# Kernel optimization log

Measured on AMD Instinct MI355X. Metric: run time of the kernel, lower is better.

## Reference

```python
import jax, jax.numpy as jnp
import numpy as np

DIM = 768
NUM_HEADS = 12
HEAD_DIM = DIM // NUM_HEADS
B, V, L = 1, 8, 512


def _block_mask_bias(V, L, dtype):
    # allowed[v_q, v_k]: views 0,1 attend to views 0,1 (incl. self); views >=2 causal (v_q >= v_k)
    vq = jnp.arange(V)[:, None]
    vk = jnp.arange(V)[None, :]
    allowed = ((vq <= 1) & (vk <= 1)) | (vq >= vk)  # [V, V]
    allowed = jnp.repeat(jnp.repeat(allowed, L, axis=0), L, axis=1)  # [V*L, V*L]
    neg_inf = jnp.asarray(-jnp.inf, dtype)
    return jnp.where(allowed, jnp.asarray(0.0, dtype), neg_inf)


def setup_inputs() -> dict:
    key = jax.random.key(0)
    k0, k1, k2, k3, k4, k5 = jax.random.split(key, 6)
    s = 1.0 / np.sqrt(DIM)
    x = jax.random.normal(k0, (B, V, L, DIM), dtype=jnp.float32)
    Wq = jax.random.normal(k1, (DIM, DIM), dtype=jnp.float32) * s
    Wk = jax.random.normal(k2, (DIM, DIM), dtype=jnp.float32) * s
    Wv = jax.random.normal(k3, (DIM, DIM), dtype=jnp.float32) * s
    Wo = jax.random.normal(k4, (DIM, DIM), dtype=jnp.float32) * s
    bo = jax.random.normal(k5, (DIM,), dtype=jnp.float32) * 0.01
    return {"x": x, "Wq": Wq, "Wk": Wk, "Wv": Wv, "Wo": Wo, "bo": bo}


def reference(x, Wq, Wk, Wv, Wo, bo):
    Bx, Vx, Lx, C = x.shape
    S = Vx * Lx
    H, D = NUM_HEADS, HEAD_DIM
    scale = D ** -0.5

    xf = x.reshape(Bx, S, C)
    # linear projections (no bias, qkv_bias=False), split heads -> [B, H, S, D]
    def split_heads(t):
        return t.reshape(Bx, S, H, D).transpose(0, 2, 1, 3)
    q = split_heads(xf @ Wq.T)
    k = split_heads(xf @ Wk.T)
    v = split_heads(xf @ Wv.T)

    bias = _block_mask_bias(Vx, Lx, q.dtype)  # [S, S], broadcast over B, H
    scores = jnp.einsum("bhqd,bhkd->bhqk", q, k) * scale + bias
    attn = jax.nn.softmax(scores, axis=-1)
    out = jnp.einsum("bhqk,bhkd->bhqd", attn, v)  # [B, H, S, D]
    out = out.transpose(0, 2, 1, 3).reshape(Bx, Vx, Lx, C)
    return out @ Wo.T + bo
```

## Files before the change

kernel.cpp:

```cpp
#include <hip/hip_runtime.h>

#define S_TOT 4096
#define C_DIM 768
#define QKV_LD 2304
#define NH 12
#define QSCALE 0.18033688011112042f

using f32x4  = __attribute__((ext_vector_type(4))) float;
using bf16x8 = __attribute__((ext_vector_type(8))) __bf16;

#if __has_builtin(__builtin_amdgcn_exp2f)
#define EXP2(x) __builtin_amdgcn_exp2f(x)
#else
#define EXP2(x) exp2f(x)
#endif

#define DRAIN_AND_BARRIER()                                     \
  do {                                                          \
    asm volatile("s_waitcnt vmcnt(0) lgkmcnt(0)" ::: "memory"); \
    __builtin_amdgcn_sched_barrier(0);                          \
    __syncthreads();                                            \
  } while (0)

__device__ inline unsigned short f2bf_bits(float f) {
  unsigned int u = __float_as_uint(f);
  u = (u + 0x7FFFu + ((u >> 16) & 1u)) >> 16;
  return (unsigned short)u;
}
__device__ inline __bf16 f2bf(float f) {
  unsigned short s = f2bf_bits(f);
  __bf16 b;
  __builtin_memcpy(&b, &s, 2);
  return b;
}

__device__ __forceinline__ void gl_lds16(const __bf16* g, __bf16* l) {
  __builtin_amdgcn_global_load_lds(
      (__attribute__((address_space(1))) void*)(g),
      (__attribute__((address_space(3))) void*)(l), 16, 0, 0);
}

__global__ void cvt_all(const float* __restrict__ x, const float* __restrict__ Wq,
                        const float* __restrict__ Wk, const float* __restrict__ Wv,
                        const float* __restrict__ Wo, __bf16* __restrict__ dst) {
  const int XN = S_TOT * C_DIM;
  const int WN = C_DIM * C_DIM;
  int i = (blockIdx.x * blockDim.x + threadIdx.x) * 4;
  if (i >= XN + 4 * WN) return;
  const float* src; float scale = 1.f; int off;
  if (i < XN)               { src = x;  off = i; }
  else if (i < XN + WN)     { src = Wq; off = i - XN; scale = QSCALE; }
  else if (i < XN + 2 * WN) { src = Wk; off = i - XN - WN; }
  else if (i < XN + 3 * WN) { src = Wv; off = i - XN - 2 * WN; }
  else                      { src = Wo; off = i - XN - 3 * WN; }
  float4 v = *reinterpret_cast<const float4*>(src + off);
  ushort4 o;
  o.x = f2bf_bits(v.x * scale); o.y = f2bf_bits(v.y * scale);
  o.z = f2bf_bits(v.z * scale); o.w = f2bf_bits(v.w * scale);
  *reinterpret_cast<ushort4*>(reinterpret_cast<unsigned short*>(dst) + i) = o;
}

template<bool OUT_BIAS_F32, bool SPLIT_V>
__global__ __launch_bounds__(256) void gemm128(
    const __bf16* __restrict__ A, const __bf16* __restrict__ B,
    void* __restrict__ Cv, const float* __restrict__ bias,
    __bf16* __restrict__ VtOut, int K, int ldc) {
  __shared__ __bf16 As[128][64];
  __shared__ __bf16 Bs[128][64];
  const int t = threadIdx.x, lane = t & 63, wv = t >> 6;
  const int wr = wv >> 1, wc = wv & 1;
  const int lhi = lane >> 4, llo = lane & 15;
  const int m0 = blockIdx.y * 128, n0 = blockIdx.x * 128;

  f32x4 acc[4][4];
  #pragma unroll
  for (int a = 0; a < 4; ++a)
    #pragma unroll
    for (int b = 0; b < 4; ++b) acc[a][b] = (f32x4){0.f, 0.f, 0.f, 0.f};

  for (int kt = 0; kt < K; kt += 64) {
    __syncthreads();
    #pragma unroll
    for (int n = 0; n < 4; ++n) {
      const int ci = n * 256 + wv * 64 + lane;
      const int r = ci >> 3;
      const int cc = (ci & 7) ^ (r & 7);
      gl_lds16(A + (size_t)(m0 + r) * K + kt + cc * 8, &As[0][0] + ci * 8);
      gl_lds16(B + (size_t)(n0 + r) * K + kt + cc * 8, &Bs[0][0] + ci * 8);
    }
    DRAIN_AND_BARRIER();
    #pragma unroll
    for (int kk = 0; kk < 2; ++kk) {
      bf16x8 af[4], bfr[4];
      #pragma unroll
      for (int mi = 0; mi < 4; ++mi) {
        const int row = wr * 64 + mi * 16 + llo;
        af[mi] = *reinterpret_cast<const bf16x8*>(
            &As[0][0] + row * 64 + (((kk << 2) | lhi) ^ (llo & 7)) * 8);
      }
      #pragma unroll
      for (int ni = 0; ni < 4; ++ni) {
        const int row = wc * 64 + ni * 16 + llo;
        bfr[ni] = *reinterpret_cast<const bf16x8*>(
            &Bs[0][0] + row * 64 + (((kk << 2) | lhi) ^ (llo & 7)) * 8);
      }
      #pragma unroll
      for (int mi = 0; mi < 4; ++mi)
        #pragma unroll
        for (int ni = 0; ni < 4; ++ni)
          acc[mi][ni] = __builtin_amdgcn_mfma_f32_16x16x32_bf16(af[mi], bfr[ni], acc[mi][ni], 0, 0, 0);
    }
  }

  if (SPLIT_V && n0 >= 1536) {
    const int head = (n0 - 1536 + wc * 64) >> 6;
    const int tile64 = (m0 >> 6) + wr;
    #pragma unroll
    for (int mi = 0; mi < 4; ++mi) {
      const int p = (mi >> 1) * 32 + lhi * 8 + (mi & 1) * 4;
      #pragma unroll
      for (int ni = 0; ni < 4; ++ni) {
        const int d = ni * 16 + llo;
        ushort4 o;
        o.x = f2bf_bits(acc[mi][ni][0]); o.y = f2bf_bits(acc[mi][ni][1]);
        o.z = f2bf_bits(acc[mi][ni][2]); o.w = f2bf_bits(acc[mi][ni][3]);
        uint2 u; __builtin_memcpy(&u, &o, 8);
        *reinterpret_cast<uint2*>(VtOut + ((size_t)head * 64 + d) * S_TOT + tile64 * 64 + p) = u;
      }
    }
    return;
  }

  #pragma unroll
  for (int mi = 0; mi < 4; ++mi)
    #pragma unroll
    for (int ni = 0; ni < 4; ++ni)
      #pragma unroll
      for (int i = 0; i < 4; ++i) {
        const int row = m0 + wr * 64 + mi * 16 + lhi * 4 + i;
        const int col = n0 + wc * 64 + ni * 16 + llo;
        if constexpr (OUT_BIAS_F32) {
          reinterpret_cast<float*>(Cv)[(size_t)row * ldc + col] = acc[mi][ni][i] + bias[col];
        } else {
          reinterpret_cast<__bf16*>(Cv)[(size_t)row * ldc + col] = f2bf(acc[mi][ni][i]);
        }
      }
}

__device__ __forceinline__ void decode9(int j, int& qb64, int& h, int& half, bool& split) {
  if (j < 192)      { split = true;  half = j & 1;  qb64 = 56 + ((j >> 1) & 7); h = j >> 4; }
  else if (j < 288) { int k = j - 192; split = false; half = 0; qb64 = 24 + (k & 7); h = k >> 3; }
  else if (j < 480) { int k = j - 288; split = true;  half = k & 1; qb64 = 48 + ((k >> 1) & 7); h = k >> 4; }
  else if (j < 672) { int k = j - 480; split = true;  half = k & 1; qb64 = 40 + ((k >> 1) & 7); h = k >> 4; }
  else if (j < 768) { int k = j - 672; split = false; half = 0; qb64 = 16 + (k & 7); h = k >> 3; }
  else if (j < 960) { int k = j - 768; split = true;  half = k & 1; qb64 = 32 + ((k >> 1) & 7); h = k >> 4; }
  else              { int k = j - 960; split = false; half = 0; qb64 = k & 15; h = k >> 4; }
}

__global__ __launch_bounds__(256) void attn_fused9(
    const __bf16* __restrict__ QKV, const __bf16* __restrict__ Vtp,
    __bf16* __restrict__ att, float* __restrict__ Opart,
    float* __restrict__ lpart) {
  __shared__ __bf16 Ks[3][64][64];
  __shared__ __bf16 Vs[3][64][64];
  const int t = threadIdx.x, lane = t & 63, wv = t >> 6;
  const int llo = lane & 15, hi = lane >> 4;
  const int sw = llo & 7;
  int qb64, h, half; bool split;
  decode9((int)blockIdx.x, qb64, h, half, split);
  const int vq = qb64 >> 3;
  const int kv_end = (vq <= 1) ? 1024 : (vq + 1) * 512;
  const int n_tiles = split ? (kv_end >> 7) : (kv_end >> 6);
  const int kstart = split ? half * (kv_end >> 1) : 0;
  const int q0 = qb64 * 64;
  const int myq = q0 + wv * 16 + llo;

  bf16x8 qf[2];
  {
    const __bf16* qrow = QKV + (size_t)myq * QKV_LD + h * 64;
    qf[0] = *reinterpret_cast<const bf16x8*>(qrow + hi * 8);
    qf[1] = *reinterpret_cast<const bf16x8*>(qrow + 32 + hi * 8);
  }
  asm volatile("s_waitcnt vmcnt(0)" ::: "memory");

  f32x4 Oa[4];
  #pragma unroll
  for (int dt = 0; dt < 4; ++dt) Oa[dt] = (f32x4){0.f, 0.f, 0.f, 0.f};
  float l = 0.f;

  const int ci0 = (wv * 2 + 0) * 64 + lane, r0 = ci0 >> 3, c0 = (ci0 & 7) ^ (r0 & 7);
  const int ci1 = (wv * 2 + 1) * 64 + lane, r1 = ci1 >> 3, c1 = (ci1 & 7) ^ (r1 & 7);
  const __bf16* kp0 = QKV + (size_t)(kstart + r0) * QKV_LD + C_DIM + h * 64 + c0 * 8;
  const __bf16* kp1 = QKV + (size_t)(kstart + r1) * QKV_LD + C_DIM + h * 64 + c1 * 8;
  const __bf16* vp0 = Vtp + ((size_t)h * 64 + r0) * S_TOT + kstart + c0 * 8;
  const __bf16* vp1 = Vtp + ((size_t)h * 64 + r1) * S_TOT + kstart + c1 * 8;
  __bf16* const kd0 = &Ks[0][0][0] + ci0 * 8 - lane * 8;
  __bf16* const kd1 = &Ks[0][0][0] + ci1 * 8 - lane * 8;
  __bf16* const vd0 = &Vs[0][0][0] + ci0 * 8 - lane * 8;
  __bf16* const vd1 = &Vs[0][0][0] + ci1 * 8 - lane * 8;

  auto stage = [&](int buf) {
    const size_t bo = (size_t)buf * 4096;
    gl_lds16(kp0, kd0 + bo);
    gl_lds16(vp0, vd0 + bo);
    gl_lds16(kp1, kd1 + bo);
    gl_lds16(vp1, vd1 + bo);
    kp0 += (size_t)64 * QKV_LD; kp1 += (size_t)64 * QKV_LD;
    vp0 += 64; vp1 += 64;
  };

  stage(0);
  stage(1);
  int cur = 0;
  for (int tt = 0; tt < n_tiles; ++tt) {
    if (tt + 1 < n_tiles) {
      asm volatile("s_waitcnt vmcnt(4)" ::: "memory");
    } else {
      asm volatile("s_waitcnt vmcnt(0)" ::: "memory");
    }
    __builtin_amdgcn_sched_barrier(0);
    __builtin_amdgcn_s_barrier();
    __builtin_amdgcn_sched_barrier(0);
    if (tt + 2 < n_tiles) {
      const int nxt = (cur + 2 >= 3) ? cur - 1 : cur + 2;
      stage(nxt);
    }
    const __bf16* Kb = &Ks[cur][0][0];
    const __bf16* Vb = &Vs[cur][0][0];

    f32x4 sc[4];
    #pragma unroll
    for (int nt = 0; nt < 4; ++nt) sc[nt] = (f32x4){0.f, 0.f, 0.f, 0.f};
    #pragma unroll
    for (int nt = 0; nt < 4; ++nt) {
      const __bf16* kr = Kb + (nt * 16 + llo) * 64;
      bf16x8 kf0 = *reinterpret_cast<const bf16x8*>(kr + ((hi ^ sw) * 8));
      bf16x8 kf1 = *reinterpret_cast<const bf16x8*>(kr + (((4 + hi) ^ sw) * 8));
      sc[nt] = __builtin_amdgcn_mfma_f32_16x16x32_bf16(kf0, qf[0], sc[nt], 0, 0, 0);
      sc[nt] = __builtin_amdgcn_mfma_f32_16x16x32_bf16(kf1, qf[1], sc[nt], 0, 0, 0);
    }

    float pp[4][4];
    #pragma unroll
    for (int nt = 0; nt < 4; ++nt)
      #pragma unroll
      for (int i = 0; i < 4; ++i) pp[nt][i] = EXP2(sc[nt][i]);
    float t0 = (pp[0][0] + pp[0][1]) + (pp[0][2] + pp[0][3]);
    float t1 = (pp[1][0] + pp[1][1]) + (pp[1][2] + pp[1][3]);
    float t2 = (pp[2][0] + pp[2][1]) + (pp[2][2] + pp[2][3]);
    float t3 = (pp[3][0] + pp[3][1]) + (pp[3][2] + pp[3][3]);
    l += (t0 + t1) + (t2 + t3);

    bf16x8 pf[2];
    #pragma unroll
    for (int mm = 0; mm < 2; ++mm)
      #pragma unroll
      for (int jj = 0; jj < 8; ++jj)
        pf[mm][jj] = (__bf16)pp[2 * mm + (jj >> 2)][jj & 3];

    #pragma unroll
    for (int dt = 0; dt < 4; ++dt) {
      const __bf16* vr = Vb + (dt * 16 + llo) * 64;
      #pragma unroll
      for (int mm = 0; mm < 2; ++mm) {
        bf16x8 va = *reinterpret_cast<const bf16x8*>(vr + (((mm * 4 + hi) ^ sw) * 8));
        Oa[dt] = __builtin_amdgcn_mfma_f32_16x16x32_bf16(va, pf[mm], Oa[dt], 0, 0, 0);
      }
    }
    cur = (cur + 1 == 3) ? 0 : cur + 1;
  }

  l += __shfl_xor(l, 16);
  l += __shfl_xor(l, 32);
  if (!split) {
    const float inv = 1.f / l;
    #pragma unroll
    for (int dt = 0; dt < 4; ++dt) {
      ushort4 o;
      o.x = f2bf_bits(Oa[dt][0] * inv);
      o.y = f2bf_bits(Oa[dt][1] * inv);
      o.z = f2bf_bits(Oa[dt][2] * inv);
      o.w = f2bf_bits(Oa[dt][3] * inv);
      *reinterpret_cast<ushort4*>(att + (size_t)myq * C_DIM + h * 64 + dt * 16 + hi * 4) = o;
    }
  } else {
    const int slot = ((qb64 - 32) * 12 + h) * 2 + half;
    float* Ob = Opart + (((size_t)slot * 64) + wv * 16 + llo) * 64;
    #pragma unroll
    for (int dt = 0; dt < 4; ++dt)
      *reinterpret_cast<f32x4*>(Ob + dt * 16 + hi * 4) = Oa[dt];
    if (hi == 0) lpart[slot * 64 + wv * 16 + llo] = l;
  }
}

__global__ __launch_bounds__(256) void merge9(
    const float* __restrict__ Opart, const float* __restrict__ lpart,
    __bf16* __restrict__ att) {
  const int b = blockIdx.x;
  const int qi = b / 12, h = b - qi * 12;
  const int t = threadIdx.x;
  const int r = t >> 2, d0 = (t & 3) * 16;
  const int slot0 = b * 2;
  const float* O0 = Opart + ((size_t)slot0 * 64 + r) * 64 + d0;
  const float* O1 = Opart + ((size_t)(slot0 + 1) * 64 + r) * 64 + d0;
  const float linv = 1.f / (lpart[slot0 * 64 + r] + lpart[(slot0 + 1) * 64 + r]);
  __bf16* dst = att + ((size_t)(qi + 32) * 64 + r) * C_DIM + h * 64 + d0;
  #pragma unroll
  for (int i = 0; i < 4; ++i) {
    f32x4 a = *reinterpret_cast<const f32x4*>(O0 + i * 4);
    f32x4 c = *reinterpret_cast<const f32x4*>(O1 + i * 4);
    ushort4 o;
    o.x = f2bf_bits((a[0] + c[0]) * linv);
    o.y = f2bf_bits((a[1] + c[1]) * linv);
    o.z = f2bf_bits((a[2] + c[2]) * linv);
    o.w = f2bf_bits((a[3] + c[3]) * linv);
    *reinterpret_cast<ushort4*>(dst + i * 4) = o;
  }
}

extern "C" void kernel_launch(void* const* d_in, const int* in_sizes, int n_in,
                              void* d_out, int out_size, void* d_ws, size_t ws_size,
                              hipStream_t stream) {
  const float* x  = (const float*)d_in[0];
  const float* Wq = (const float*)d_in[1];
  const float* Wk = (const float*)d_in[2];
  const float* Wv = (const float*)d_in[3];
  const float* Wo = (const float*)d_in[4];
  const float* bo = (const float*)d_in[5];

  __bf16* xb   = (__bf16*)d_ws;
  __bf16* Wqkv = xb + (size_t)S_TOT * C_DIM;
  __bf16* Wob  = Wqkv + (size_t)3 * C_DIM * C_DIM;
  __bf16* QKV  = Wob + (size_t)C_DIM * C_DIM;
  __bf16* Vtp  = QKV + (size_t)S_TOT * QKV_LD;
  __bf16* att  = Vtp + (size_t)NH * 64 * S_TOT;
  float*  Opart = (float*)(att + (size_t)S_TOT * C_DIM);
  float*  lpart = Opart + (size_t)768 * 64 * 64;

  {
    const int tot = S_TOT * C_DIM + 4 * C_DIM * C_DIM;
    cvt_all<<<dim3((tot / 4 + 255) / 256), dim3(256), 0, stream>>>(
        x, Wq, Wk, Wv, Wo, xb);
  }

  gemm128<false, true><<<dim3(QKV_LD / 128, S_TOT / 128), dim3(256), 0, stream>>>(
      xb, Wqkv, (void*)QKV, nullptr, Vtp, C_DIM, QKV_LD);

  attn_fused9<<<dim3(1152), dim3(256), 0, stream>>>(QKV, Vtp, att, Opart, lpart);

  merge9<<<dim3(384), dim3(256), 0, stream>>>(Opart, lpart, att);

  gemm128<true, false><<<dim3(C_DIM / 128, S_TOT / 128), dim3(256), 0, stream>>>(
      att, Wob, d_out, bo, nullptr, C_DIM, C_DIM);
}
```

Measured before the change: 101.2 us.

## Rebalance attention split-KV work and load V fragments directly from global

Replaces the two-way KV split with a finer partition so every query block, not only the later views, is split into chunks of roughly 12-16 KV tiles, raising the attention grid from 1152 to 1920 blocks. The V projection is written in a pre-swizzled fragment layout so each lane reads its MFMA operands straight from global memory into registers, dropping the V LDS staging buffer and half of the async copies. The merge kernel now combines 2-4 partials per query block. This trades more partial-output traffic and a larger merge for better load balance and lower LDS use, with V reads now exposed to global latency inside the loop.

```diff
diff --git a/kernel.cpp b/kernel.cpp
--- a/kernel.cpp
+++ b/kernel.cpp
@@ -64,7 +64,7 @@
 __global__ __launch_bounds__(256) void gemm128(
     const __bf16* __restrict__ A, const __bf16* __restrict__ B,
     void* __restrict__ Cv, const float* __restrict__ bias,
-    __bf16* __restrict__ VtOut, int K, int ldc) {
+    __bf16* __restrict__ V2, int K, int ldc) {
   __shared__ __bf16 As[128][64];
   __shared__ __bf16 Bs[128][64];
   const int t = threadIdx.x, lane = t & 63, wv = t >> 6;
@@ -114,10 +114,10 @@
 
   if (SPLIT_V && n0 >= 1536) {
     const int head = (n0 - 1536 + wc * 64) >> 6;
-    const int tile64 = (m0 >> 6) + wr;
+    const int T = (m0 >> 6) + wr;
     #pragma unroll
     for (int mi = 0; mi < 4; ++mi) {
-      const int p = (mi >> 1) * 32 + lhi * 8 + (mi & 1) * 4;
+      const int c = (mi >> 1) * 4 + lhi;
       #pragma unroll
       for (int ni = 0; ni < 4; ++ni) {
         const int d = ni * 16 + llo;
@@ -125,7 +125,8 @@
         o.x = f2bf_bits(acc[mi][ni][0]); o.y = f2bf_bits(acc[mi][ni][1]);
         o.z = f2bf_bits(acc[mi][ni][2]); o.w = f2bf_bits(acc[mi][ni][3]);
         uint2 u; __builtin_memcpy(&u, &o, 8);
-        *reinterpret_cast<uint2*>(VtOut + ((size_t)head * 64 + d) * S_TOT + tile64 * 64 + p) = u;
+        *reinterpret_cast<uint2*>(
+            V2 + ((((size_t)head * 64 + T) * 8 + c) * 64 + d) * 8 + (mi & 1) * 4) = u;
       }
     }
     return;
@@ -147,31 +148,49 @@
       }
 }
 
-__device__ __forceinline__ void decode9(int j, int& qb64, int& h, int& half, bool& split) {
-  if (j < 192)      { split = true;  half = j & 1;  qb64 = 56 + ((j >> 1) & 7); h = j >> 4; }
-  else if (j < 288) { int k = j - 192; split = false; half = 0; qb64 = 24 + (k & 7); h = k >> 3; }
-  else if (j < 480) { int k = j - 288; split = true;  half = k & 1; qb64 = 48 + ((k >> 1) & 7); h = k >> 4; }
-  else if (j < 672) { int k = j - 480; split = true;  half = k & 1; qb64 = 40 + ((k >> 1) & 7); h = k >> 4; }
-  else if (j < 768) { int k = j - 672; split = false; half = 0; qb64 = 16 + (k & 7); h = k >> 3; }
-  else if (j < 960) { int k = j - 768; split = true;  half = k & 1; qb64 = 32 + ((k >> 1) & 7); h = k >> 4; }
-  else              { int k = j - 960; split = false; half = 0; qb64 = k & 15; h = k >> 4; }
-}
-
-__global__ __launch_bounds__(256) void attn_fused9(
-    const __bf16* __restrict__ QKV, const __bf16* __restrict__ Vtp,
+__device__ __forceinline__ void decode10(int j, int& qb64, int& h, int& nt,
+                                         int& kstart, int& slot) {
+  if (j < 384) {
+    const int c = j & 3, q = (j >> 2) & 7; h = j >> 5;
+    qb64 = 56 + q; nt = 16; kstart = c * 1024;
+    slot = ((q * 12) + h) * 4 + c;
+  } else if (j < 672) {
+    const int k = j - 384, c = k % 3, k3 = k / 3, q = k3 & 7; h = k3 >> 3;
+    qb64 = 40 + q; nt = 16; kstart = c * 1024;
+    slot = 768 + ((q * 12) + h) * 3 + c;
+  } else if (j < 864) {
+    const int k = j - 672, c = k & 1, q = (k >> 1) & 7; h = k >> 4;
+    qb64 = 24 + q; nt = 16; kstart = c * 1024;
+    slot = 1344 + ((q * 12) + h) * 2 + c;
+  } else if (j < 1056) {
+    const int k = j - 864;
+    qb64 = k & 15; h = k >> 4; nt = 16; kstart = 0; slot = -1;
+  } else if (j < 1440) {
+    const int k = j - 1056, c = k & 3, q = (k >> 2) & 7; h = k >> 5;
+    qb64 = 48 + q; nt = 14; kstart = c * 896;
+    slot = 384 + ((q * 12) + h) * 4 + c;
+  } else if (j < 1728) {
+    const int k = j - 1440, c = k % 3, k3 = k / 3, q = k3 & 7; h = k3 >> 3;
+    qb64 = 32 + q; nt = (c == 0) ? 14 : 13;
+    kstart = (c == 0) ? 0 : (896 + (c - 1) * 832);
+    slot = 1056 + ((q * 12) + h) * 3 + c;
+  } else {
+    const int k = j - 1728, c = k & 1, q = (k >> 1) & 7; h = k >> 4;
+    qb64 = 16 + q; nt = 12; kstart = c * 768;
+    slot = 1536 + ((q * 12) + h) * 2 + c;
+  }
+}
+
+__global__ __launch_bounds__(256) void attn_fused10(
+    const __bf16* __restrict__ QKV, const __bf16* __restrict__ V2,
     __bf16* __restrict__ att, float* __restrict__ Opart,
     float* __restrict__ lpart) {
   __shared__ __bf16 Ks[3][64][64];
-  __shared__ __bf16 Vs[3][64][64];
   const int t = threadIdx.x, lane = t & 63, wv = t >> 6;
   const int llo = lane & 15, hi = lane >> 4;
   const int sw = llo & 7;
-  int qb64, h, half; bool split;
-  decode9((int)blockIdx.x, qb64, h, half, split);
-  const int vq = qb64 >> 3;
-  const int kv_end = (vq <= 1) ? 1024 : (vq + 1) * 512;
-  const int n_tiles = split ? (kv_end >> 7) : (kv_end >> 6);
-  const int kstart = split ? half * (kv_end >> 1) : 0;
+  int qb64, h, n_tiles, kstart, slot;
+  decode10((int)blockIdx.x, qb64, h, n_tiles, kstart, slot);
   const int q0 = qb64 * 64;
   const int myq = q0 + wv * 16 + llo;
 
@@ -192,41 +211,44 @@
   const int ci1 = (wv * 2 + 1) * 64 + lane, r1 = ci1 >> 3, c1 = (ci1 & 7) ^ (r1 & 7);
   const __bf16* kp0 = QKV + (size_t)(kstart + r0) * QKV_LD + C_DIM + h * 64 + c0 * 8;
   const __bf16* kp1 = QKV + (size_t)(kstart + r1) * QKV_LD + C_DIM + h * 64 + c1 * 8;
-  const __bf16* vp0 = Vtp + ((size_t)h * 64 + r0) * S_TOT + kstart + c0 * 8;
-  const __bf16* vp1 = Vtp + ((size_t)h * 64 + r1) * S_TOT + kstart + c1 * 8;
-  __bf16* const kd0 = &Ks[0][0][0] + ci0 * 8 - lane * 8;
-  __bf16* const kd1 = &Ks[0][0][0] + ci1 * 8 - lane * 8;
-  __bf16* const vd0 = &Vs[0][0][0] + ci0 * 8 - lane * 8;
-  __bf16* const vd1 = &Vs[0][0][0] + ci1 * 8 - lane * 8;
+  __bf16* const kd0 = &Ks[0][0][0] + (wv * 2 + 0) * 512;
+  __bf16* const kd1 = &Ks[0][0][0] + (wv * 2 + 1) * 512;
 
   auto stage = [&](int buf) {
     const size_t bo = (size_t)buf * 4096;
     gl_lds16(kp0, kd0 + bo);
-    gl_lds16(vp0, vd0 + bo);
     gl_lds16(kp1, kd1 + bo);
-    gl_lds16(vp1, vd1 + bo);
     kp0 += (size_t)64 * QKV_LD; kp1 += (size_t)64 * QKV_LD;
-    vp0 += 64; vp1 += 64;
   };
+
+  const __bf16* vg = V2 + ((size_t)(h * 64 + (kstart >> 6))) * 4096 + hi * 512 + llo * 8;
 
   stage(0);
   stage(1);
   int cur = 0;
   for (int tt = 0; tt < n_tiles; ++tt) {
     if (tt + 1 < n_tiles) {
-      asm volatile("s_waitcnt vmcnt(4)" ::: "memory");
+      asm volatile("s_waitcnt vmcnt(2)" ::: "memory");
     } else {
       asm volatile("s_waitcnt vmcnt(0)" ::: "memory");
     }
     __builtin_amdgcn_sched_barrier(0);
     __builtin_amdgcn_s_barrier();
     __builtin_amdgcn_sched_barrier(0);
+
+    bf16x8 va[4][2];
+    #pragma unroll
+    for (int dt = 0; dt < 4; ++dt)
+      #pragma unroll
+      for (int mm = 0; mm < 2; ++mm)
+        va[dt][mm] = *reinterpret_cast<const bf16x8*>(vg + mm * 2048 + dt * 128);
+    __builtin_amdgcn_sched_barrier(0);
+
     if (tt + 2 < n_tiles) {
       const int nxt = (cur + 2 >= 3) ? cur - 1 : cur + 2;
       stage(nxt);
     }
     const __bf16* Kb = &Ks[cur][0][0];
-    const __bf16* Vb = &Vs[cur][0][0];
 
     f32x4 sc[4];
     #pragma unroll
@@ -259,20 +281,18 @@
         pf[mm][jj] = (__bf16)pp[2 * mm + (jj >> 2)][jj & 3];
 
     #pragma unroll
-    for (int dt = 0; dt < 4; ++dt) {
-      const __bf16* vr = Vb + (dt * 16 + llo) * 64;
-      #pragma unroll
-      for (int mm = 0; mm < 2; ++mm) {
-        bf16x8 va = *reinterpret_cast<const bf16x8*>(vr + (((mm * 4 + hi) ^ sw) * 8));
-        Oa[dt] = __builtin_amdgcn_mfma_f32_16x16x32_bf16(va, pf[mm], Oa[dt], 0, 0, 0);
-      }
-    }
+    for (int dt = 0; dt < 4; ++dt)
+      #pragma unroll
+      for (int mm = 0; mm < 2; ++mm)
+        Oa[dt] = __builtin_amdgcn_mfma_f32_16x16x32_bf16(va[dt][mm], pf[mm], Oa[dt], 0, 0, 0);
+
+    vg += 4096;
     cur = (cur + 1 == 3) ? 0 : cur + 1;
   }
 
   l += __shfl_xor(l, 16);
   l += __shfl_xor(l, 32);
-  if (!split) {
+  if (slot < 0) {
     const float inv = 1.f / l;
     #pragma unroll
     for (int dt = 0; dt < 4; ++dt) {
@@ -284,7 +304,6 @@
       *reinterpret_cast<ushort4*>(att + (size_t)myq * C_DIM + h * 64 + dt * 16 + hi * 4) = o;
     }
   } else {
-    const int slot = ((qb64 - 32) * 12 + h) * 2 + half;
     float* Ob = Opart + (((size_t)slot * 64) + wv * 16 + llo) * 64;
     #pragma unroll
     for (int dt = 0; dt < 4; ++dt)
@@ -293,27 +312,41 @@
   }
 }
 
-__global__ __launch_bounds__(256) void merge9(
+__global__ __launch_bounds__(256) void merge10(
     const float* __restrict__ Opart, const float* __restrict__ lpart,
     __bf16* __restrict__ att) {
   const int b = blockIdx.x;
   const int qi = b / 12, h = b - qi * 12;
+  const int qb64 = 16 + qi;
+  int base, n;
+  if      (qb64 >= 56) { n = 4; base = ((qb64 - 56) * 12 + h) * 4; }
+  else if (qb64 >= 48) { n = 4; base = 384 + ((qb64 - 48) * 12 + h) * 4; }
+  else if (qb64 >= 40) { n = 3; base = 768 + ((qb64 - 40) * 12 + h) * 3; }
+  else if (qb64 >= 32) { n = 3; base = 1056 + ((qb64 - 32) * 12 + h) * 3; }
+  else if (qb64 >= 24) { n = 2; base = 1344 + ((qb64 - 24) * 12 + h) * 2; }
+  else                 { n = 2; base = 1536 + ((qb64 - 16) * 12 + h) * 2; }
   const int t = threadIdx.x;
   const int r = t >> 2, d0 = (t & 3) * 16;
-  const int slot0 = b * 2;
-  const float* O0 = Opart + ((size_t)slot0 * 64 + r) * 64 + d0;
-  const float* O1 = Opart + ((size_t)(slot0 + 1) * 64 + r) * 64 + d0;
-  const float linv = 1.f / (lpart[slot0 * 64 + r] + lpart[(slot0 + 1) * 64 + r]);
-  __bf16* dst = att + ((size_t)(qi + 32) * 64 + r) * C_DIM + h * 64 + d0;
+  f32x4 s[4] = {{0.f,0.f,0.f,0.f},{0.f,0.f,0.f,0.f},{0.f,0.f,0.f,0.f},{0.f,0.f,0.f,0.f}};
+  float L = 0.f;
+  for (int k = 0; k < n; ++k) {
+    const float* O = Opart + ((size_t)(base + k) * 64 + r) * 64 + d0;
+    #pragma unroll
+    for (int i = 0; i < 4; ++i) {
+      f32x4 v = *reinterpret_cast<const f32x4*>(O + i * 4);
+      s[i][0] += v[0]; s[i][1] += v[1]; s[i][2] += v[2]; s[i][3] += v[3];
+    }
+    L += lpart[(base + k) * 64 + r];
+  }
+  const float linv = 1.f / L;
+  __bf16* dst = att + ((size_t)qb64 * 64 + r) * C_DIM + h * 64 + d0;
   #pragma unroll
   for (int i = 0; i < 4; ++i) {
-    f32x4 a = *reinterpret_cast<const f32x4*>(O0 + i * 4);
-    f32x4 c = *reinterpret_cast<const f32x4*>(O1 + i * 4);
     ushort4 o;
-    o.x = f2bf_bits((a[0] + c[0]) * linv);
-    o.y = f2bf_bits((a[1] + c[1]) * linv);
-    o.z = f2bf_bits((a[2] + c[2]) * linv);
-    o.w = f2bf_bits((a[3] + c[3]) * linv);
+    o.x = f2bf_bits(s[i][0] * linv);
+    o.y = f2bf_bits(s[i][1] * linv);
+    o.z = f2bf_bits(s[i][2] * linv);
+    o.w = f2bf_bits(s[i][3] * linv);
     *reinterpret_cast<ushort4*>(dst + i * 4) = o;
   }
 }
@@ -332,10 +365,10 @@
   __bf16* Wqkv = xb + (size_t)S_TOT * C_DIM;
   __bf16* Wob  = Wqkv + (size_t)3 * C_DIM * C_DIM;
   __bf16* QKV  = Wob + (size_t)C_DIM * C_DIM;
-  __bf16* Vtp  = QKV + (size_t)S_TOT * QKV_LD;
-  __bf16* att  = Vtp + (size_t)NH * 64 * S_TOT;
+  __bf16* V2   = QKV + (size_t)S_TOT * QKV_LD;
+  __bf16* att  = V2 + (size_t)NH * 64 * S_TOT;
   float*  Opart = (float*)(att + (size_t)S_TOT * C_DIM);
-  float*  lpart = Opart + (size_t)768 * 64 * 64;
+  float*  lpart = Opart + (size_t)1728 * 64 * 64;
 
   {
     const int tot = S_TOT * C_DIM + 4 * C_DIM * C_DIM;
@@ -344,11 +377,11 @@
   }
 
   gemm128<false, true><<<dim3(QKV_LD / 128, S_TOT / 128), dim3(256), 0, stream>>>(
-      xb, Wqkv, (void*)QKV, nullptr, Vtp, C_DIM, QKV_LD);
-
-  attn_fused9<<<dim3(1152), dim3(256), 0, stream>>>(QKV, Vtp, att, Opart, lpart);
-
-  merge9<<<dim3(384), dim3(256), 0, stream>>>(Opart, lpart, att);
+      xb, Wqkv, (void*)QKV, nullptr, V2, C_DIM, QKV_LD);
+
+  attn_fused10<<<dim3(1920), dim3(256), 0, stream>>>(QKV, V2, att, Opart, lpart);
+
+  merge10<<<dim3(576), dim3(256), 0, stream>>>(Opart, lpart, att);
 
   gemm128<true, false><<<dim3(C_DIM / 128, S_TOT / 128), dim3(256), 0, stream>>>(
       att, Wob, d_out, bo, nullptr, C_DIM, C_DIM);
```

Result: slower. 104.5 us (+3.2%).
